# Performance work log

Measured on AMD Instinct MI355X. Metric: run time of the kernel, lower is better.

The kernel has to match this reference:

```python
import jax, jax.numpy as jnp
import numpy as np

DIM = 256
H = 4
K = 16
R = 4
EPS = 1e-5


def _conv1x1(x, W, b):
    # x: [B, Cin, N, P], W: [Cout, Cin], b: [Cout]
    return jnp.einsum('oc,bcnp->bonp', W, x) + b[None, :, None, None]


def setup_inputs() -> dict:
    key = jax.random.key(0)
    ks = jax.random.split(key, 12)
    B, N = 4, 8192
    s = 1.0 / np.sqrt(DIM)
    inp = {
        'queries': jax.random.normal(ks[0], (B, DIM, N, R), dtype=jnp.float32),
        'feats': jax.random.normal(ks[1], (B, DIM, N, K), dtype=jnp.float32),
        'Wq': jax.random.normal(ks[2], (DIM, DIM), dtype=jnp.float32) * s,
        'bq': jnp.zeros((DIM,), dtype=jnp.float32),
        'Wk': jax.random.normal(ks[3], (DIM, DIM), dtype=jnp.float32) * s,
        'bk': jnp.zeros((DIM,), dtype=jnp.float32),
        'Wv': jax.random.normal(ks[4], (DIM, DIM), dtype=jnp.float32) * s,
        'bv': jnp.zeros((DIM,), dtype=jnp.float32),
        'W1': jax.random.normal(ks[5], (2 * DIM, DIM), dtype=jnp.float32) * s,
        'b1': jnp.zeros((2 * DIM,), dtype=jnp.float32),
        'gamma': jnp.ones((2 * DIM,), dtype=jnp.float32),
        'beta': jnp.zeros((2 * DIM,), dtype=jnp.float32),
        'W2': jax.random.normal(ks[6], (DIM, 2 * DIM), dtype=jnp.float32) * (1.0 / np.sqrt(2 * DIM)),
        'b2': jnp.zeros((DIM,), dtype=jnp.float32),
    }
    return inp


def reference(queries, feats, Wq, bq, Wk, bk, Wv, bv, W1, b1, gamma, beta, W2, b2):
    B, _, N, _ = feats.shape
    d = DIM // H
    queries_iden = queries  # [B, dim, N, r]

    q = _conv1x1(queries, Wq, bq).reshape(B, H, d, N, R)   # [B,h,d,N,r]
    k = _conv1x1(feats, Wk, bk).reshape(B, H, d, N, K)     # [B,h,d,N,K]
    v = _conv1x1(feats, Wv, bv).reshape(B, H, d, N, K)     # [B,h,d,N,K]

    # logits: [B,N,h,r,K]
    logits = jnp.einsum('bhdnr,bhdnk->bnhrk', q, k) * (d ** -0.5)
    soft = jax.nn.softmax(logits, axis=-1)
    # agg: [B,N,h,r,d] -> permute to [B,N,h,d,r] -> [B,N,dim,r] -> [B,dim,N,r]
    agg = jnp.einsum('bnhrk,bhdnk->bnhdr', soft, v)
    agg = agg.reshape(B, N, DIM, R).transpose(0, 2, 1, 3)
    agg = agg + queries_iden

    # FFN: conv1x1 -> BN (training-mode batch stats) -> ReLU -> conv1x1, residual, ReLU
    h1 = _conv1x1(agg, W1, b1)  # [B, 2*dim, N, r]
    mean = jnp.mean(h1, axis=(0, 2, 3), keepdims=True)
    var = jnp.var(h1, axis=(0, 2, 3), keepdims=True)
    h1 = (h1 - mean) * jax.lax.rsqrt(var + EPS)
    h1 = h1 * gamma[None, :, None, None] + beta[None, :, None, None]
    h1 = jax.nn.relu(h1)
    h2 = _conv1x1(h1, W2, b2)
    return jax.nn.relu(h2 + agg)
```

## Files before the change

kernel.cpp:

```cpp
#include <hip/hip_runtime.h>
#include <hip/hip_bf16.h>

#define NB 4
#define NRQ 32768
#define NKF 131072

using u16 = unsigned short;
typedef short bf16x8 __attribute__((ext_vector_type(8)));
typedef float f32x4  __attribute__((ext_vector_type(4)));
typedef u16   u16x8  __attribute__((ext_vector_type(8)));
typedef u16   u16x4  __attribute__((ext_vector_type(4)));
typedef u16   u16x2  __attribute__((ext_vector_type(2)));

#if defined(__has_builtin)
#  if __has_builtin(__builtin_amdgcn_fdot2_f32_bf16)
#    define HAVE_DOT2 1
#  endif
#endif
#ifndef HAVE_DOT2
#  define HAVE_DOT2 0
#endif

#if HAVE_DOT2
typedef __bf16 bfv2 __attribute__((ext_vector_type(2)));
union bpack  { bf16x8 v; bfv2 p[4]; };
union bpack4 { u16x4  v; bfv2 p[2]; };
__device__ __forceinline__ float dot2(bfv2 a, bfv2 b, float c){
  return __builtin_amdgcn_fdot2_f32_bf16(a, b, c, false);
}
#endif
union vpack  { bf16x8 v; u16 e[8]; };
union vpack4 { u16x4 v; u16 e[4]; };

__device__ __forceinline__ u16 f2b(float f){
  __hip_bfloat16 h = __float2bfloat16(f);
  return *reinterpret_cast<u16*>(&h);
}
__device__ __forceinline__ float b2f(u16 v){
  return __uint_as_float(((unsigned)v) << 16);
}

#define GLOAD16(g, l) __builtin_amdgcn_global_load_lds( \
    (const __attribute__((address_space(1))) unsigned int*)(g), \
    (__attribute__((address_space(3))) unsigned int*)(l), 16, 0, 0)

__global__ __launch_bounds__(256) void cvtW_k(
    const float* __restrict__ Wk, const float* __restrict__ Wv,
    const float* __restrict__ Wq, const float* __restrict__ W1,
    const float* __restrict__ W2, u16* __restrict__ wT,
    const float* __restrict__ bk, const float* __restrict__ bv,
    float* __restrict__ bKV, float* __restrict__ stats)
{
  if (blockIdx.x >= 224){
    int i = (blockIdx.x - 224) * 256 + threadIdx.x;
    if (i < 512)       bKV[i] = (i < 256) ? bk[i] : bv[i - 256];
    else if (i < 1536) stats[i - 512] = 0.f;
    return;
  }
  long e = ((long)blockIdx.x * 256 + threadIdx.x) * 8;
  const float* src; long off;
  if      (e < 65536)  { src = Wk; off = e; }
  else if (e < 131072) { src = Wv; off = e - 65536; }
  else if (e < 196608) { src = Wq; off = e - 131072; }
  else if (e < 327680) { src = W1; off = e - 196608; }
  else                 { src = W2; off = e - 327680; }
  float4 f0 = *reinterpret_cast<const float4*>(src + off);
  float4 f1 = *reinterpret_cast<const float4*>(src + off + 4);
  u16x8 p;
  p[0]=f2b(f0.x); p[1]=f2b(f0.y); p[2]=f2b(f0.z); p[3]=f2b(f0.w);
  p[4]=f2b(f1.x); p[5]=f2b(f1.y); p[6]=f2b(f1.z); p[7]=f2b(f1.w);
  *reinterpret_cast<u16x8*>(wT + e) = p;
}

__global__ __launch_bounds__(256) void transpose_k(
    const float* __restrict__ in, u16* __restrict__ out,
    int NCtot, long outBatch)
{
  __shared__ u16 sT[64][264];
  const int t = threadIdx.x, b = blockIdx.y;
  const int nr0 = blockIdx.x * 64;
  const int cb = t >> 2, nrq = t & 3;
  const long ib = (long)b * 256 * NCtot + nr0;

  #pragma unroll
  for (int ci = 0; ci < 4; ++ci){
    const int c = cb + ci * 64;
    const float* src = in + ib + (long)c * NCtot + nrq * 16;
    #pragma unroll
    for (int j = 0; j < 4; ++j){
      float4 f = *reinterpret_cast<const float4*>(src + j * 4);
      int nr = nrq * 16 + j * 4;
      sT[nr+0][c] = f2b(f.x); sT[nr+1][c] = f2b(f.y);
      sT[nr+2][c] = f2b(f.z); sT[nr+3][c] = f2b(f.w);
    }
  }
  __syncthreads();
  const int row = t >> 2, qtr = t & 3;
  u16* orow = out + (long)b * outBatch + (long)(nr0 + row) * 256 + qtr * 64;
  #pragma unroll
  for (int i = 0; i < 8; ++i)
    *reinterpret_cast<u16x8*>(orow + i * 8) =
        *reinterpret_cast<const u16x8*>(&sT[row][qtr * 64 + i * 8]);
}

template<int MODE, int KD>
__global__ __launch_bounds__(256) void gemm_k(
    const u16* __restrict__ A, long aBatch, int chTiles,
    const u16* __restrict__ Wb, const float* __restrict__ bias,
    u16* __restrict__ outH, long oBatch, int NCH,
    float* __restrict__ statSum, float* __restrict__ statSq,
    const float* __restrict__ xsc, const float* __restrict__ xsh,
    const u16* __restrict__ residT,
    float* __restrict__ outF, long fBatch)
{
  __shared__ __align__(16) char sA[2][16384];
  __shared__ __align__(16) char sB[2][16384];

  const int t = threadIdx.x, lane = t & 63, wid = t >> 6;
  const int wm = wid >> 1, wn = wid & 1;
  const int b = blockIdx.z;

  const int nwg = gridDim.x, orig = blockIdx.x;
  const int qq = nwg >> 3, rr = nwg & 7, xcd = orig & 7, pos = orig >> 3;
  const int wg = (xcd < rr ? xcd * (qq + 1) : rr * (qq + 1) + (xcd - rr) * qq) + pos;
  const int rowT = wg / chTiles, chT = wg % chTiles;

  const u16* Ab = A + (long)b * aBatch + (long)rowT * 128 * KD;
  const u16* Wt = Wb + (long)chT * 128 * KD;
  const int sub = lane >> 3, kc8 = ((lane & 7) ^ sub) * 8;

  f32x4 acc[4][4];
  #pragma unroll
  for (int i = 0; i < 4; ++i)
    #pragma unroll
    for (int j = 0; j < 4; ++j) acc[i][j] = (f32x4){0.f,0.f,0.f,0.f};

  auto STAGE = [&](int buf, int ks){
    const int k0 = ks * 64;
    if constexpr (MODE == 3){
      const int wrow = t >> 1, whalf = t & 1;
      const u16* arow = Ab + (long)wrow * KD + k0 + whalf * 32;
      #pragma unroll
      for (int i = 0; i < 4; ++i){
        u16x8 v = *reinterpret_cast<const u16x8*>(arow + i * 8);
        const int kb = k0 + whalf*32 + i*8;
        float4 s0 = *reinterpret_cast<const float4*>(xsc + kb);
        float4 s1 = *reinterpret_cast<const float4*>(xsc + kb + 4);
        float4 h0 = *reinterpret_cast<const float4*>(xsh + kb);
        float4 h1 = *reinterpret_cast<const float4*>(xsh + kb + 4);
        u16x8 o;
        o[0]=f2b(fmaxf(b2f(v[0])*s0.x+h0.x,0.f));
        o[1]=f2b(fmaxf(b2f(v[1])*s0.y+h0.y,0.f));
        o[2]=f2b(fmaxf(b2f(v[2])*s0.z+h0.z,0.f));
        o[3]=f2b(fmaxf(b2f(v[3])*s0.w+h0.w,0.f));
        o[4]=f2b(fmaxf(b2f(v[4])*s1.x+h1.x,0.f));
        o[5]=f2b(fmaxf(b2f(v[5])*s1.y+h1.y,0.f));
        o[6]=f2b(fmaxf(b2f(v[6])*s1.z+h1.z,0.f));
        o[7]=f2b(fmaxf(b2f(v[7])*s1.w+h1.w,0.f));
        *reinterpret_cast<u16x8*>(
            sA[buf] + ((wrow*128 + whalf*64 + i*16) ^ ((wrow & 7) << 4))) = o;
      }
      #pragma unroll
      for (int i = 0; i < 4; ++i){
        const int chunk = wid * 4 + i;
        GLOAD16(Wt + (long)(chunk*8 + sub)*KD + k0 + kc8, sB[buf] + chunk*1024);
      }
    } else {
      #pragma unroll
      for (int i = 0; i < 4; ++i){
        const int chunk = wid * 4 + i;
        GLOAD16(Ab + (long)(chunk*8 + sub)*KD + k0 + kc8, sA[buf] + chunk*1024);
        GLOAD16(Wt + (long)(chunk*8 + sub)*KD + k0 + kc8, sB[buf] + chunk*1024);
      }
    }
  };

  constexpr int NT = KD / 64;
  STAGE(0, 0);
  __syncthreads();
  int cur = 0;
  for (int ks = 0; ks < NT; ++ks){
    if (ks + 1 < NT) STAGE(cur ^ 1, ks + 1);
    const char* pA = sA[cur]; const char* pB = sB[cur];
    #pragma unroll
    for (int kk = 0; kk < 2; ++kk){
      bf16x8 af[4], bf[4];
      #pragma unroll
      for (int mi = 0; mi < 4; ++mi){
        int m = wm*64 + mi*16 + (lane & 15);
        af[mi] = *reinterpret_cast<const bf16x8*>(
            pA + ((m*128 + kk*64 + (lane>>4)*16) ^ ((m & 7) << 4)));
      }
      #pragma unroll
      for (int ni = 0; ni < 4; ++ni){
        int c = wn*64 + ni*16 + (lane & 15);
        bf[ni] = *reinterpret_cast<const bf16x8*>(
            pB + ((c*128 + kk*64 + (lane>>4)*16) ^ ((c & 7) << 4)));
      }
      #pragma unroll
      for (int mi = 0; mi < 4; ++mi)
        #pragma unroll
        for (int ni = 0; ni < 4; ++ni)
          acc[mi][ni] = __builtin_amdgcn_mfma_f32_16x16x32_bf16(
              af[mi], bf[ni], acc[mi][ni], 0, 0, 0);
    }
    __syncthreads();
    cur ^= 1;
  }

  int chI[4]; float bv[4];
  #pragma unroll
  for (int ni = 0; ni < 4; ++ni){
    int ch = chT*128 + wn*64 + ni*16 + (lane & 15);
    chI[ni] = ch;
    bv[ni] = bias[ch];
  }
  if (MODE != 3){
    float s[4] = {0,0,0,0}, sq[4] = {0,0,0,0};
    u16* outb = outH + (long)b * oBatch;
    #pragma unroll
    for (int mi = 0; mi < 4; ++mi){
      #pragma unroll
      for (int j = 0; j < 4; ++j){
        const long row = rowT*128 + wm*64 + mi*16 + (lane>>4)*4 + j;
        #pragma unroll
        for (int ni = 0; ni < 4; ++ni){
          float v = acc[mi][ni][j] + bv[ni];
          outb[row * NCH + chI[ni]] = f2b(v);
          if (MODE == 1){ s[ni] += v; sq[ni] += v * v; }
        }
      }
    }
    if (MODE == 1){
      #pragma unroll
      for (int ni = 0; ni < 4; ++ni){
        s[ni]  += __shfl_xor(s[ni], 16);  s[ni]  += __shfl_xor(s[ni], 32);
        sq[ni] += __shfl_xor(sq[ni], 16); sq[ni] += __shfl_xor(sq[ni], 32);
      }
      if (lane < 16){
        #pragma unroll
        for (int ni = 0; ni < 4; ++ni){
          atomicAdd(&statSum[chI[ni]], s[ni]);
          atomicAdd(&statSq[chI[ni]],  sq[ni]);
        }
      }
    }
  } else {
    const u16* rb = residT + (long)b * ((long)NRQ * 256);
    #pragma unroll
    for (int mi = 0; mi < 4; ++mi){
      const int nr0 = rowT*128 + wm*64 + mi*16 + (lane>>4)*4;
      #pragma unroll
      for (int ni = 0; ni < 4; ++ni){
        float4 o;
        o.x = fmaxf(acc[mi][ni][0] + bv[ni] + b2f(rb[(long)(nr0+0)*256 + chI[ni]]), 0.f);
        o.y = fmaxf(acc[mi][ni][1] + bv[ni] + b2f(rb[(long)(nr0+1)*256 + chI[ni]]), 0.f);
        o.z = fmaxf(acc[mi][ni][2] + bv[ni] + b2f(rb[(long)(nr0+2)*256 + chI[ni]]), 0.f);
        o.w = fmaxf(acc[mi][ni][3] + bv[ni] + b2f(rb[(long)(nr0+3)*256 + chI[ni]]), 0.f);
        *reinterpret_cast<float4*>(outF + (long)b*fBatch + (long)chI[ni]*NRQ + nr0) = o;
      }
    }
  }
}

__global__ __launch_bounds__(512, 2) void kvattn_k(
    const float* __restrict__ feats, const u16* __restrict__ wKV,
    const float* __restrict__ bKV, const u16* __restrict__ qT,
    const u16* __restrict__ qrT, u16* __restrict__ aggT)
{
  __shared__ __align__(16) char LDS[142848];
  char*  sAg = LDS;
  char*  sW  = LDS + 18432;
  char*  sK  = LDS;
  char*  sV  = LDS + 67584;
  float* sSf = (float*)(LDS + 134144);

  const int t = threadIdx.x, lane = t & 63, wid = t >> 6;
  const int wr = wid >> 2, wc = wid & 3;
  const int b = blockIdx.y;
  const long row0 = (long)blockIdx.x * 128;

  const int chL = t >> 4, nq = t & 15;
  const float* fbase = feats + (long)b * 256 * NKF + row0 + nq;

  auto STAGEW = [&](int buf, int ks){
    const int k0 = ks * 32;
    #pragma unroll
    for (int i = 0; i < 4; ++i){
      const int cw = wid * 4 + i;
      const int ch = cw * 16 + (lane >> 2), jd = lane & 3;
      GLOAD16(wKV + (long)ch * 256 + k0 + ((jd ^ ((ch >> 1) & 3)) * 8),
              sW + buf * 32768 + cw * 1024);
    }
  };
  auto LOADA = [&](int ks, float* ar){
    const float* src = fbase + (long)(ks * 32 + chL) * NKF;
    #pragma unroll
    for (int i = 0; i < 8; ++i) ar[i] = src[16 * i];
  };
  auto WRITEA = [&](int buf, const float* ar){
    #pragma unroll
    for (int i = 0; i < 8; ++i){
      const int r = nq + 16 * i;
      *reinterpret_cast<u16*>(sAg + buf*9216 + r*72 + chL*2) = f2b(ar[i]);
    }
  };

  f32x4 acc[4][8];
  #pragma unroll
  for (int i = 0; i < 4; ++i)
    #pragma unroll
    for (int j = 0; j < 8; ++j) acc[i][j] = (f32x4){0.f,0.f,0.f,0.f};

  float aR[8];
  {
    LOADA(0, aR);
    STAGEW(0, 0);
    WRITEA(0, aR);
  }
  __syncthreads();

  int cur = 0;
  const int jq = lane >> 4;
  #pragma unroll
  for (int ks = 0; ks < 8; ++ks){
    if (ks < 7){
      LOADA(ks + 1, aR);
      STAGEW(cur ^ 1, ks + 1);
    }
    const char* pA = sAg + cur * 9216;
    const char* pW = sW  + cur * 32768;
    bf16x8 af[4];
    #pragma unroll
    for (int mi = 0; mi < 4; ++mi){
      const int m = wr*64 + mi*16 + (lane & 15);
      af[mi] = *reinterpret_cast<const bf16x8*>(pA + m*72 + jq*16);
    }
    __builtin_amdgcn_s_setprio(1);
    #pragma unroll
    for (int ni = 0; ni < 8; ++ni){
      const int ch = wc*128 + ni*16 + (lane & 15);
      bf16x8 bf = *reinterpret_cast<const bf16x8*>(
          pW + ch*64 + (((jq ^ ((ch>>1)&3)) * 16)));
      #pragma unroll
      for (int mi = 0; mi < 4; ++mi)
        acc[mi][ni] = __builtin_amdgcn_mfma_f32_16x16x32_bf16(
            af[mi], bf, acc[mi][ni], 0, 0, 0);
    }
    __builtin_amdgcn_s_setprio(0);
    if (ks < 7) WRITEA(cur ^ 1, aR);
    __syncthreads();
    cur ^= 1;
  }

  {
    float bv[8];
    #pragma unroll
    for (int ni = 0; ni < 8; ++ni) bv[ni] = bKV[wc*128 + ni*16 + (lane & 15)];
    char* dst = (wc < 2) ? sK : sV;
    const int pitch = (wc < 2) ? 528 : 520;
    const int chb = (wc & 1) * 128;
    #pragma unroll
    for (int mi = 0; mi < 4; ++mi){
      #pragma unroll
      for (int ni = 0; ni < 8; ++ni){
        const int ch = chb + ni*16 + (lane & 15);
        #pragma unroll
        for (int j = 0; j < 4; ++j){
          const int r = wr*64 + mi*16 + (lane>>4)*4 + j;
          *reinterpret_cast<u16*>(dst + r*pitch + ch*2) =
              f2b(acc[mi][ni][j] + bv[ni]);
        }
      }
    }
  }

  const int p = wid;
  const int nqg = blockIdx.x * 8 + p;
  const int c0 = lane * 4;
  u16x4 rq[4];
  {
    const u16* rqp = qrT + ((long)b*NRQ + (long)nqg*4)*256 + c0;
    #pragma unroll
    for (int r = 0; r < 4; ++r)
      rq[r] = *reinterpret_cast<const u16x4*>(rqp + r*256);
  }
  __syncthreads();

  {
    const int h = lane >> 4, kk = lane & 15;
    const u16* qb = qT + ((long)b*NRQ + (long)nqg*4)*256 + h*64;
    const char* kr = sK + (p*16 + kk)*528 + h*128;
    float l[4] = {0.f, 0.f, 0.f, 0.f};
#if HAVE_DOT2
    #pragma unroll
    for (int d8 = 0; d8 < 8; ++d8){
      bpack K8;
      K8.v = *reinterpret_cast<const bf16x8*>(kr + d8*16);
      #pragma unroll
      for (int r = 0; r < 4; ++r){
        bpack Q;
        Q.v = *reinterpret_cast<const bf16x8*>(qb + r*256 + d8*8);
        #pragma unroll
        for (int pi = 0; pi < 4; ++pi) l[r] = dot2(K8.p[pi], Q.p[pi], l[r]);
      }
    }
#else
    #pragma unroll
    for (int d8 = 0; d8 < 8; ++d8){
      vpack K8;
      K8.v = *reinterpret_cast<const bf16x8*>(kr + d8*16);
      #pragma unroll
      for (int r = 0; r < 4; ++r){
        vpack Q;
        Q.v = *reinterpret_cast<const bf16x8*>(qb + r*256 + d8*8);
        #pragma unroll
        for (int e = 0; e < 8; ++e) l[r] = fmaf(b2f(K8.e[e]), b2f(Q.e[e]), l[r]);
      }
    }
#endif
    float4 prob;
    #pragma unroll
    for (int r = 0; r < 4; ++r){
      float x = l[r] * 0.125f;
      float m = x;
      #pragma unroll
      for (int off = 1; off < 16; off <<= 1) m = fmaxf(m, __shfl_xor(m, off));
      float e = __expf(x - m);
      float ssum = e;
      #pragma unroll
      for (int off = 1; off < 16; off <<= 1) ssum += __shfl_xor(ssum, off);
      float pr = e / ssum;
      if (r == 0) prob.x = pr; else if (r == 1) prob.y = pr;
      else if (r == 2) prob.z = pr; else prob.w = pr;
    }
    *reinterpret_cast<float4*>(sSf + (p*4 + h)*68 + kk*4) = prob;
  }
  __syncthreads();

  {
    const int h = c0 >> 6;
    const char* vrow = sV + (p*16)*520;
    const float* ss = sSf + (p*4 + h)*68;
    float a[4][4] = {};
    #pragma unroll
    for (int kk = 0; kk < 16; ++kk){
      vpack4 vv;
      vv.v = *reinterpret_cast<const u16x4*>(vrow + kk*520 + c0*2);
      float4 sv = *reinterpret_cast<const float4*>(ss + kk*4);
      #pragma unroll
      for (int cc = 0; cc < 4; ++cc){
        float vf = b2f(vv.e[cc]);
        a[0][cc] += sv.x*vf; a[1][cc] += sv.y*vf;
        a[2][cc] += sv.z*vf; a[3][cc] += sv.w*vf;
      }
    }
    u16* ob = aggT + ((long)b*NRQ + (long)nqg*4)*256 + c0;
    #pragma unroll
    for (int r = 0; r < 4; ++r){
      u16x4 pk;
      #pragma unroll
      for (int cc = 0; cc < 4; ++cc) pk[cc] = f2b(a[r][cc] + b2f(rq[r][cc]));
      *reinterpret_cast<u16x4*>(ob + r*256) = pk;
    }
  }
}

__global__ void finalize_k(const float* __restrict__ st,
                           const float* __restrict__ gamma,
                           const float* __restrict__ beta,
                           float* __restrict__ out)
{
  int o = blockIdx.x*256 + threadIdx.x;
  const float inv = 1.f / 131072.f;
  float mean = st[o] * inv;
  float var  = st[512 + o] * inv - mean*mean;
  float sc   = gamma[o] * rsqrtf(var + 1e-5f);
  out[o]       = sc;
  out[512 + o] = beta[o] - mean * sc;
}

extern "C" void kernel_launch(void* const* d_in, const int* in_sizes, int n_in,
                              void* d_out, int out_size, void* d_ws, size_t ws_size,
                              hipStream_t stream)
{
  (void)in_sizes; (void)n_in; (void)out_size; (void)ws_size;
  const float* queries = (const float*)d_in[0];
  const float* feats   = (const float*)d_in[1];
  const float* Wq = (const float*)d_in[2];
  const float* bq = (const float*)d_in[3];
  const float* Wk = (const float*)d_in[4];
  const float* bk = (const float*)d_in[5];
  const float* Wv = (const float*)d_in[6];
  const float* bv = (const float*)d_in[7];
  const float* W1 = (const float*)d_in[8];
  const float* b1 = (const float*)d_in[9];
  const float* gamma = (const float*)d_in[10];
  const float* beta  = (const float*)d_in[11];
  const float* W2 = (const float*)d_in[12];
  const float* b2 = (const float*)d_in[13];

  char* ws = (char*)d_ws;
  u16*   h1T   = (u16*)ws;
  u16*   qrT   = (u16*)(ws + 134217728L);
  u16*   qT    = (u16*)(ws + 201326592L);
  u16*   aggT  = (u16*)(ws + 268435456L);
  float* stats = (float*)(ws + 335544320L);
  float* scale = stats + 1024;
  float* shift = stats + 1536;
  u16*   wT    = (u16*)(ws + 335552512L);
  u16*   wKV   = wT;
  u16*   wQ    = wT + 131072;
  u16*   wW1   = wT + 196608;
  u16*   wW2   = wT + 327680;
  float* bKV   = (float*)(wT + 458752);

  cvtW_k<<<dim3(230), 256, 0, stream>>>(Wk, Wv, Wq, W1, W2, wT,
                                        bk, bv, bKV, stats);

  transpose_k<<<dim3(NRQ/64, NB), 256, 0, stream>>>(queries, qrT, NRQ, (long)NRQ*256);

  gemm_k<0, 256><<<dim3(512, 1, NB), 256, 0, stream>>>(
      qrT, (long)NRQ*256, 2, wQ, bq,
      qT, (long)NRQ*256, 256, nullptr, nullptr, nullptr, nullptr,
      nullptr, nullptr, 0);

  kvattn_k<<<dim3(NKF/128, NB), 512, 0, stream>>>(
      feats, wKV, bKV, qT, qrT, aggT);

  gemm_k<1, 256><<<dim3(1024, 1, NB), 256, 0, stream>>>(
      aggT, (long)NRQ*256, 4, wW1, b1,
      h1T, (long)NRQ*512, 512, stats, stats + 512, nullptr, nullptr,
      nullptr, nullptr, 0);

  finalize_k<<<dim3(2), 256, 0, stream>>>(stats, gamma, beta, scale);

  gemm_k<3, 512><<<dim3(512, 1, NB), 256, 0, stream>>>(
      h1T, (long)NRQ*512, 2, wW2, b2,
      nullptr, 0, 256, nullptr, nullptr, scale, shift,
      aggT, (float*)d_out, (long)256*NRQ);
}
```

Baseline: 657.8 us.

## Split fused KV-projection+attention into GEMM plus separate attention kernel

```diff
diff --git a/kernel.cpp b/kernel.cpp
--- a/kernel.cpp
+++ b/kernel.cpp
@@ -10,7 +10,6 @@
 typedef float f32x4  __attribute__((ext_vector_type(4)));
 typedef u16   u16x8  __attribute__((ext_vector_type(8)));
 typedef u16   u16x4  __attribute__((ext_vector_type(4)));
-typedef u16   u16x2  __attribute__((ext_vector_type(2)));
 
 #if defined(__has_builtin)
 #  if __has_builtin(__builtin_amdgcn_fdot2_f32_bf16)
@@ -23,8 +22,7 @@
 
 #if HAVE_DOT2
 typedef __bf16 bfv2 __attribute__((ext_vector_type(2)));
-union bpack  { bf16x8 v; bfv2 p[4]; };
-union bpack4 { u16x4  v; bfv2 p[2]; };
+union bpack { bf16x8 v; bfv2 p[4]; };
 __device__ __forceinline__ float dot2(bfv2 a, bfv2 b, float c){
   return __builtin_amdgcn_fdot2_f32_bf16(a, b, c, false);
 }
@@ -72,37 +70,6 @@
   *reinterpret_cast<u16x8*>(wT + e) = p;
 }
 
-__global__ __launch_bounds__(256) void transpose_k(
-    const float* __restrict__ in, u16* __restrict__ out,
-    int NCtot, long outBatch)
-{
-  __shared__ u16 sT[64][264];
-  const int t = threadIdx.x, b = blockIdx.y;
-  const int nr0 = blockIdx.x * 64;
-  const int cb = t >> 2, nrq = t & 3;
-  const long ib = (long)b * 256 * NCtot + nr0;
-
-  #pragma unroll
-  for (int ci = 0; ci < 4; ++ci){
-    const int c = cb + ci * 64;
-    const float* src = in + ib + (long)c * NCtot + nrq * 16;
-    #pragma unroll
-    for (int j = 0; j < 4; ++j){
-      float4 f = *reinterpret_cast<const float4*>(src + j * 4);
-      int nr = nrq * 16 + j * 4;
-      sT[nr+0][c] = f2b(f.x); sT[nr+1][c] = f2b(f.y);
-      sT[nr+2][c] = f2b(f.z); sT[nr+3][c] = f2b(f.w);
-    }
-  }
-  __syncthreads();
-  const int row = t >> 2, qtr = t & 3;
-  u16* orow = out + (long)b * outBatch + (long)(nr0 + row) * 256 + qtr * 64;
-  #pragma unroll
-  for (int i = 0; i < 8; ++i)
-    *reinterpret_cast<u16x8*>(orow + i * 8) =
-        *reinterpret_cast<const u16x8*>(&sT[row][qtr * 64 + i * 8]);
-}
-
 template<int MODE, int KD>
 __global__ __launch_bounds__(256) void gemm_k(
     const u16* __restrict__ A, long aBatch, int chTiles,
@@ -110,6 +77,7 @@
     u16* __restrict__ outH, long oBatch, int NCH,
     float* __restrict__ statSum, float* __restrict__ statSq,
     const float* __restrict__ xsc, const float* __restrict__ xsh,
+    const float* __restrict__ Afp, long afpBatch, long aStride,
     const u16* __restrict__ residT,
     float* __restrict__ outF, long fBatch)
 {
@@ -165,6 +133,26 @@
         const int chunk = wid * 4 + i;
         GLOAD16(Wt + (long)(chunk*8 + sub)*KD + k0 + kc8, sB[buf] + chunk*1024);
       }
+    } else if constexpr (MODE == 4){
+      const int chq = lane;
+      const float* qsrc = Afp + (long)b * afpBatch
+                        + (long)(k0 + chq) * aStride + (long)rowT * 128 + wid * 32;
+      #pragma unroll
+      for (int i = 0; i < 8; ++i){
+        float4 f = *reinterpret_cast<const float4*>(qsrc + i * 4);
+        #pragma unroll
+        for (int j = 0; j < 4; ++j){
+          const int m = wid*32 + i*4 + j;
+          float e = (j == 0) ? f.x : (j == 1) ? f.y : (j == 2) ? f.z : f.w;
+          *reinterpret_cast<u16*>(
+              sA[buf] + ((m*128 + chq*2) ^ ((m & 7) << 4))) = f2b(e);
+        }
+      }
+      #pragma unroll
+      for (int i = 0; i < 4; ++i){
+        const int chunk = wid * 4 + i;
+        GLOAD16(Wt + (long)(chunk*8 + sub)*KD + k0 + kc8, sB[buf] + chunk*1024);
+      }
     } else {
       #pragma unroll
       for (int i = 0; i < 4; ++i){
@@ -263,140 +251,35 @@
   }
 }
 
-__global__ __launch_bounds__(512, 2) void kvattn_k(
-    const float* __restrict__ feats, const u16* __restrict__ wKV,
-    const float* __restrict__ bKV, const u16* __restrict__ qT,
-    const u16* __restrict__ qrT, u16* __restrict__ aggT)
+__global__ __launch_bounds__(256) void attn_k(
+    const u16* __restrict__ kvB, const u16* __restrict__ qT,
+    const float* __restrict__ queries, u16* __restrict__ aggT)
 {
-  __shared__ __align__(16) char LDS[142848];
-  char*  sAg = LDS;
-  char*  sW  = LDS + 18432;
-  char*  sK  = LDS;
-  char*  sV  = LDS + 67584;
-  float* sSf = (float*)(LDS + 134144);
-
-  const int t = threadIdx.x, lane = t & 63, wid = t >> 6;
-  const int wr = wid >> 2, wc = wid & 3;
+  __shared__ float sSf[16 * 68];
+  const int t = threadIdx.x, lane = t & 63, p = t >> 6;
   const int b = blockIdx.y;
-  const long row0 = (long)blockIdx.x * 128;
-
-  const int chL = t >> 4, nq = t & 15;
-  const float* fbase = feats + (long)b * 256 * NKF + row0 + nq;
-
-  auto STAGEW = [&](int buf, int ks){
-    const int k0 = ks * 32;
-    #pragma unroll
-    for (int i = 0; i < 4; ++i){
-      const int cw = wid * 4 + i;
-      const int ch = cw * 16 + (lane >> 2), jd = lane & 3;
-      GLOAD16(wKV + (long)ch * 256 + k0 + ((jd ^ ((ch >> 1) & 3)) * 8),
-              sW + buf * 32768 + cw * 1024);
-    }
-  };
-  auto LOADA = [&](int ks, float* ar){
-    const float* src = fbase + (long)(ks * 32 + chL) * NKF;
-    #pragma unroll
-    for (int i = 0; i < 8; ++i) ar[i] = src[16 * i];
-  };
-  auto WRITEA = [&](int buf, const float* ar){
-    #pragma unroll
-    for (int i = 0; i < 8; ++i){
-      const int r = nq + 16 * i;
-      *reinterpret_cast<u16*>(sAg + buf*9216 + r*72 + chL*2) = f2b(ar[i]);
-    }
-  };
-
-  f32x4 acc[4][8];
+  const long nqg = (long)blockIdx.x * 4 + p;
+  const u16* kvb = kvB + ((long)b * NKF + nqg * 16) * 512;
+
+  const int c0 = lane * 4;
+  float qr[4][4];
   #pragma unroll
-  for (int i = 0; i < 4; ++i)
-    #pragma unroll
-    for (int j = 0; j < 8; ++j) acc[i][j] = (f32x4){0.f,0.f,0.f,0.f};
-
-  float aR[8];
-  {
-    LOADA(0, aR);
-    STAGEW(0, 0);
-    WRITEA(0, aR);
-  }
-  __syncthreads();
-
-  int cur = 0;
-  const int jq = lane >> 4;
-  #pragma unroll
-  for (int ks = 0; ks < 8; ++ks){
-    if (ks < 7){
-      LOADA(ks + 1, aR);
-      STAGEW(cur ^ 1, ks + 1);
-    }
-    const char* pA = sAg + cur * 9216;
-    const char* pW = sW  + cur * 32768;
-    bf16x8 af[4];
-    #pragma unroll
-    for (int mi = 0; mi < 4; ++mi){
-      const int m = wr*64 + mi*16 + (lane & 15);
-      af[mi] = *reinterpret_cast<const bf16x8*>(pA + m*72 + jq*16);
-    }
-    __builtin_amdgcn_s_setprio(1);
-    #pragma unroll
-    for (int ni = 0; ni < 8; ++ni){
-      const int ch = wc*128 + ni*16 + (lane & 15);
-      bf16x8 bf = *reinterpret_cast<const bf16x8*>(
-          pW + ch*64 + (((jq ^ ((ch>>1)&3)) * 16)));
-      #pragma unroll
-      for (int mi = 0; mi < 4; ++mi)
-        acc[mi][ni] = __builtin_amdgcn_mfma_f32_16x16x32_bf16(
-            af[mi], bf, acc[mi][ni], 0, 0, 0);
-    }
-    __builtin_amdgcn_s_setprio(0);
-    if (ks < 7) WRITEA(cur ^ 1, aR);
-    __syncthreads();
-    cur ^= 1;
-  }
-
-  {
-    float bv[8];
-    #pragma unroll
-    for (int ni = 0; ni < 8; ++ni) bv[ni] = bKV[wc*128 + ni*16 + (lane & 15)];
-    char* dst = (wc < 2) ? sK : sV;
-    const int pitch = (wc < 2) ? 528 : 520;
-    const int chb = (wc & 1) * 128;
-    #pragma unroll
-    for (int mi = 0; mi < 4; ++mi){
-      #pragma unroll
-      for (int ni = 0; ni < 8; ++ni){
-        const int ch = chb + ni*16 + (lane & 15);
-        #pragma unroll
-        for (int j = 0; j < 4; ++j){
-          const int r = wr*64 + mi*16 + (lane>>4)*4 + j;
-          *reinterpret_cast<u16*>(dst + r*pitch + ch*2) =
-              f2b(acc[mi][ni][j] + bv[ni]);
-        }
-      }
-    }
-  }
-
-  const int p = wid;
-  const int nqg = blockIdx.x * 8 + p;
-  const int c0 = lane * 4;
-  u16x4 rq[4];
-  {
-    const u16* rqp = qrT + ((long)b*NRQ + (long)nqg*4)*256 + c0;
-    #pragma unroll
-    for (int r = 0; r < 4; ++r)
-      rq[r] = *reinterpret_cast<const u16x4*>(rqp + r*256);
-  }
-  __syncthreads();
+  for (int cc = 0; cc < 4; ++cc){
+    float4 q4 = *reinterpret_cast<const float4*>(
+        queries + ((long)b*256 + c0 + cc) * NRQ + nqg * 4);
+    qr[cc][0]=q4.x; qr[cc][1]=q4.y; qr[cc][2]=q4.z; qr[cc][3]=q4.w;
+  }
 
   {
     const int h = lane >> 4, kk = lane & 15;
-    const u16* qb = qT + ((long)b*NRQ + (long)nqg*4)*256 + h*64;
-    const char* kr = sK + (p*16 + kk)*528 + h*128;
+    const u16* kr = kvb + kk*512 + h*64;
+    const u16* qb = qT + ((long)b*NRQ + nqg*4)*256 + h*64;
     float l[4] = {0.f, 0.f, 0.f, 0.f};
 #if HAVE_DOT2
     #pragma unroll
     for (int d8 = 0; d8 < 8; ++d8){
       bpack K8;
-      K8.v = *reinterpret_cast<const bf16x8*>(kr + d8*16);
+      K8.v = *reinterpret_cast<const bf16x8*>(kr + d8*8);
       #pragma unroll
       for (int r = 0; r < 4; ++r){
         bpack Q;
@@ -409,7 +292,7 @@
     #pragma unroll
     for (int d8 = 0; d8 < 8; ++d8){
       vpack K8;
-      K8.v = *reinterpret_cast<const bf16x8*>(kr + d8*16);
+      K8.v = *reinterpret_cast<const bf16x8*>(kr + d8*8);
       #pragma unroll
       for (int r = 0; r < 4; ++r){
         vpack Q;
@@ -440,13 +323,13 @@
 
   {
     const int h = c0 >> 6;
-    const char* vrow = sV + (p*16)*520;
+    const u16* vb = kvb + 256 + c0;
     const float* ss = sSf + (p*4 + h)*68;
     float a[4][4] = {};
     #pragma unroll
     for (int kk = 0; kk < 16; ++kk){
       vpack4 vv;
-      vv.v = *reinterpret_cast<const u16x4*>(vrow + kk*520 + c0*2);
+      vv.v = *reinterpret_cast<const u16x4*>(vb + kk*512);
       float4 sv = *reinterpret_cast<const float4*>(ss + kk*4);
       #pragma unroll
       for (int cc = 0; cc < 4; ++cc){
@@ -455,12 +338,12 @@
         a[2][cc] += sv.z*vf; a[3][cc] += sv.w*vf;
       }
     }
-    u16* ob = aggT + ((long)b*NRQ + (long)nqg*4)*256 + c0;
+    u16* ob = aggT + ((long)b*NRQ + nqg*4)*256 + c0;
     #pragma unroll
     for (int r = 0; r < 4; ++r){
       u16x4 pk;
       #pragma unroll
-      for (int cc = 0; cc < 4; ++cc) pk[cc] = f2b(a[r][cc] + b2f(rq[r][cc]));
+      for (int cc = 0; cc < 4; ++cc) pk[cc] = f2b(a[r][cc] + qr[cc][r]);
       *reinterpret_cast<u16x4*>(ob + r*256) = pk;
     }
   }
@@ -501,14 +384,14 @@
   const float* b2 = (const float*)d_in[13];
 
   char* ws = (char*)d_ws;
+  u16*   kvB   = (u16*)ws;
   u16*   h1T   = (u16*)ws;
-  u16*   qrT   = (u16*)(ws + 134217728L);
-  u16*   qT    = (u16*)(ws + 201326592L);
-  u16*   aggT  = (u16*)(ws + 268435456L);
-  float* stats = (float*)(ws + 335544320L);
+  u16*   qT    = (u16*)(ws + 536870912L);
+  u16*   aggT  = (u16*)(ws + 603979776L);
+  float* stats = (float*)(ws + 671088640L);
   float* scale = stats + 1024;
   float* shift = stats + 1536;
-  u16*   wT    = (u16*)(ws + 335552512L);
+  u16*   wT    = (u16*)(ws + 671096832L);
   u16*   wKV   = wT;
   u16*   wQ    = wT + 131072;
   u16*   wW1   = wT + 196608;
@@ -518,25 +401,27 @@
   cvtW_k<<<dim3(230), 256, 0, stream>>>(Wk, Wv, Wq, W1, W2, wT,
                                         bk, bv, bKV, stats);
 
-  transpose_k<<<dim3(NRQ/64, NB), 256, 0, stream>>>(queries, qrT, NRQ, (long)NRQ*256);
-
-  gemm_k<0, 256><<<dim3(512, 1, NB), 256, 0, stream>>>(
-      qrT, (long)NRQ*256, 2, wQ, bq,
+  gemm_k<4, 256><<<dim3(512, 1, NB), 256, 0, stream>>>(
+      nullptr, 0, 2, wQ, bq,
       qT, (long)NRQ*256, 256, nullptr, nullptr, nullptr, nullptr,
-      nullptr, nullptr, 0);
-
-  kvattn_k<<<dim3(NKF/128, NB), 512, 0, stream>>>(
-      feats, wKV, bKV, qT, qrT, aggT);
+      queries, (long)256*NRQ, NRQ, nullptr, nullptr, 0);
+
+  gemm_k<4, 256><<<dim3(4096, 1, NB), 256, 0, stream>>>(
+      nullptr, 0, 4, wKV, bKV,
+      kvB, (long)NKF*512, 512, nullptr, nullptr, nullptr, nullptr,
+      feats, (long)256*NKF, NKF, nullptr, nullptr, 0);
+
+  attn_k<<<dim3(NKF/64, NB), 256, 0, stream>>>(kvB, qT, queries, aggT);
 
   gemm_k<1, 256><<<dim3(1024, 1, NB), 256, 0, stream>>>(
       aggT, (long)NRQ*256, 4, wW1, b1,
       h1T, (long)NRQ*512, 512, stats, stats + 512, nullptr, nullptr,
-      nullptr, nullptr, 0);
+      nullptr, 0, 0, nullptr, nullptr, 0);
 
   finalize_k<<<dim3(2), 256, 0, stream>>>(stats, gamma, beta, scale);
 
   gemm_k<3, 512><<<dim3(512, 1, NB), 256, 0, stream>>>(
       h1T, (long)NRQ*512, 2, wW2, b2,
       nullptr, 0, 256, nullptr, nullptr, scale, shift,
-      aggT, (float*)d_out, (long)256*NRQ);
-}
+      nullptr, 0, 0, aggT, (float*)d_out, (long)256*NRQ);
+}
```

Result: slower. 1.008 ms (+53.3%).
